# Kernel tuning notes

Hardware: AMD Instinct MI355X
Metric: run time of the kernel (lower is better)

The kernel has to match this reference:

```python
import jax, jax.numpy as jnp
import numpy as np

B, Hh, Ww, C, D = 32, 14, 14, 512, 8192

def setup_inputs() -> dict:
    key = jax.random.key(0)
    k1, k2, k3, k4, k5, k6 = jax.random.split(key, 6)
    bottom1 = jax.random.normal(k1, (B, Hh, Ww, C), dtype=jnp.float32)
    bottom2 = jax.random.normal(k2, (B, Hh, Ww, C), dtype=jnp.float32)
    # rand_s: random +/-1 (trainable weights in the original layer)
    rand_s_1 = (2.0 * jax.random.randint(k3, (C,), 0, 2).astype(jnp.float32) - 1.0)
    rand_s_2 = (2.0 * jax.random.randint(k4, (C,), 0, 2).astype(jnp.float32) - 1.0)
    # rand_h: hash bucket index in [0, D) per input channel (fixed, non-trainable)
    rand_h_1 = jax.random.randint(k5, (C,), 0, D, dtype=jnp.int32)
    rand_h_2 = jax.random.randint(k6, (C,), 0, D, dtype=jnp.int32)
    return {"bottom1": bottom1, "bottom2": bottom2,
            "rand_s_1": rand_s_1, "rand_s_2": rand_s_2,
            "rand_h_1": rand_h_1, "rand_h_2": rand_h_2}

def _count_sketch(x_flat, rand_s, rand_h, out_dim):
    # x_flat: [N, C]. Equivalent to x_flat @ sparse_sketch_matrix [C, out_dim]
    # where sketch[c, rand_h[c]] = rand_s[c].
    z = x_flat * rand_s                                   # [N, C]
    # scatter-add channels into their hash buckets along the feature axis
    return jax.ops.segment_sum(z.T, rand_h, num_segments=out_dim).T  # [N, D]

def reference(bottom1, bottom2, rand_s_1, rand_s_2, rand_h_1, rand_h_2):
    b, h, w, c1 = bottom1.shape
    c2 = bottom2.shape[-1]
    x1 = bottom1.reshape(-1, c1)
    x2 = bottom2.reshape(-1, c2)
    sk1 = _count_sketch(x1, rand_s_1, rand_h_1, D)        # [N, D]
    sk2 = _count_sketch(x2, rand_s_2, rand_h_2, D)        # [N, D]
    fft1 = jnp.fft.fft(sk1.astype(jnp.complex64), axis=-1)
    fft2 = jnp.fft.fft(sk2.astype(jnp.complex64), axis=-1)
    cbp_flat = jnp.real(jnp.fft.ifft(fft1 * fft2, axis=-1))  # circular conv
    cbp = cbp_flat.reshape(b, h, w, D)
    return jnp.sum(cbp, axis=(1, 2))                      # [B, D]
```

## Files before the change

kernel.cpp:

```cpp
#include <hip/hip_runtime.h>


#define NB   32
#define HW   196
#define CC   512
#define DD   8192
#define NTHR 256
#define TILES_PER_B 16

typedef __attribute__((ext_vector_type(8)))  __bf16 bf8;
typedef __attribute__((ext_vector_type(16))) float  f32x16;

__global__ __launch_bounds__(NTHR) void cbp_mfma_kernel(
    const float* __restrict__ x1, const float* __restrict__ x2,
    const float* __restrict__ s1, const float* __restrict__ s2,
    const int*   __restrict__ h1, const int*   __restrict__ h2,
    float* __restrict__ ws, float* __restrict__ out, int use_ws)
{
    __shared__ float accD[DD];

    const int bid  = blockIdx.x;
    const int b    = bid >> 4;
    const int t1   = (bid >> 2) & 3;
    const int t2   = bid & 3;
    const int tid  = threadIdx.x;
    const int wid  = tid >> 6;
    const int lane = tid & 63;
    const int wr   = wid >> 1;
    const int wc   = wid & 1;
    const int lo5  = lane & 31;
    const int hi   = lane >> 5;

    for (int i = tid; i < DD; i += NTHR) accD[i] = 0.0f;
    __syncthreads();

    const int c1w = t1 * 128 + wr * 64;
    const int c2w = t2 * 128 + wc * 64;

    const float* A0 = x1 + (size_t)b * HW * CC + (c1w + lo5);
    const float* A1 = A0 + 32;
    const float* B0 = x2 + (size_t)b * HW * CC + (c2w + lo5);
    const float* B1 = B0 + 32;

    f32x16 acc00 = {}, acc01 = {}, acc10 = {}, acc11 = {};

    for (int ks = 0; ks < 12; ++ks) {
        const int kb = ks * 16 + hi * 8;
        bf8 a0, a1, b0v, b1v;
        #pragma unroll
        for (int j = 0; j < 8; ++j) {
            const size_t off = (size_t)(kb + j) * CC;
            a0[j]  = (__bf16)A0[off];
            a1[j]  = (__bf16)A1[off];
            b0v[j] = (__bf16)B0[off];
            b1v[j] = (__bf16)B1[off];
        }
        acc00 = __builtin_amdgcn_mfma_f32_32x32x16_bf16(a0, b0v, acc00, 0, 0, 0);
        acc01 = __builtin_amdgcn_mfma_f32_32x32x16_bf16(a0, b1v, acc01, 0, 0, 0);
        acc10 = __builtin_amdgcn_mfma_f32_32x32x16_bf16(a1, b0v, acc10, 0, 0, 0);
        acc11 = __builtin_amdgcn_mfma_f32_32x32x16_bf16(a1, b1v, acc11, 0, 0, 0);
    }
    {
        const int kb = 192 + hi * 8;
        bf8 a0, a1, b0v, b1v;
        #pragma unroll
        for (int j = 0; j < 8; ++j) {
            const int k = kb + j;
            const size_t off = (size_t)k * CC;
            const bool v = (k < HW);
            a0[j]  = (__bf16)(v ? A0[off] : 0.0f);
            a1[j]  = (__bf16)(v ? A1[off] : 0.0f);
            b0v[j] = (__bf16)(v ? B0[off] : 0.0f);
            b1v[j] = (__bf16)(v ? B1[off] : 0.0f);
        }
        acc00 = __builtin_amdgcn_mfma_f32_32x32x16_bf16(a0, b0v, acc00, 0, 0, 0);
        acc01 = __builtin_amdgcn_mfma_f32_32x32x16_bf16(a0, b1v, acc01, 0, 0, 0);
        acc10 = __builtin_amdgcn_mfma_f32_32x32x16_bf16(a1, b0v, acc10, 0, 0, 0);
        acc11 = __builtin_amdgcn_mfma_f32_32x32x16_bf16(a1, b1v, acc11, 0, 0, 0);
    }

    const float s2v0 = s2[c2w + lo5];
    const float s2v1 = s2[c2w + 32 + lo5];
    const int   h2v0 = h2[c2w + lo5];
    const int   h2v1 = h2[c2w + 32 + lo5];

    #pragma unroll
    for (int rt = 0; rt < 2; ++rt) {
        const f32x16 accL = rt ? acc10 : acc00;
        const f32x16 accR = rt ? acc11 : acc01;
        #pragma unroll
        for (int reg = 0; reg < 16; ++reg) {
            const int c1 = c1w + rt * 32 + (reg & 3) + 8 * (reg >> 2) + 4 * hi;
            const float sv = s1[c1];
            const int   hv = h1[c1];
            atomicAdd(&accD[(hv + h2v0) & (DD - 1)], sv * s2v0 * accL[reg]);
            atomicAdd(&accD[(hv + h2v1) & (DD - 1)], sv * s2v1 * accR[reg]);
        }
    }
    __syncthreads();

    if (use_ws) {
        float4* dst = (float4*)(ws + (size_t)bid * DD);
        const float4* src = (const float4*)accD;
        #pragma unroll
        for (int i = 0; i < DD / 4 / NTHR; ++i)
            dst[tid + i * NTHR] = src[tid + i * NTHR];
    } else {
        float* ob = out + (size_t)b * DD;
        for (int i = tid; i < DD; i += NTHR)
            atomicAdd(&ob[i], accD[i]);
    }
}

__global__ __launch_bounds__(NTHR) void cbp_reduce_kernel(
    const float* __restrict__ ws, float* __restrict__ out)
{
    const int b   = blockIdx.x >> 3;
    const int d0  = (blockIdx.x & 7) * 1024 + threadIdx.x * 4;
    const float* base = ws + (size_t)b * TILES_PER_B * DD + d0;
    float4 sum = {0.f, 0.f, 0.f, 0.f};
    #pragma unroll
    for (int t = 0; t < TILES_PER_B; ++t) {
        float4 v = *(const float4*)(base + (size_t)t * DD);
        sum.x += v.x; sum.y += v.y; sum.z += v.z; sum.w += v.w;
    }
    *(float4*)(out + (size_t)b * DD + d0) = sum;
}

extern "C" void kernel_launch(void* const* d_in, const int* in_sizes, int n_in,
                              void* d_out, int out_size, void* d_ws, size_t ws_size,
                              hipStream_t stream) {
    const float* x1 = (const float*)d_in[0];
    const float* x2 = (const float*)d_in[1];
    const float* s1 = (const float*)d_in[2];
    const float* s2 = (const float*)d_in[3];
    const int*   h1 = (const int*)d_in[4];
    const int*   h2 = (const int*)d_in[5];
    float* out = (float*)d_out;
    float* ws  = (float*)d_ws;

    const size_t need = (size_t)NB * TILES_PER_B * DD * sizeof(float);
    const int use_ws = (ws_size >= need) ? 1 : 0;

    if (!use_ws) {
        hipMemsetAsync(out, 0, (size_t)out_size * sizeof(float), stream);
    }

    dim3 grid(NB * TILES_PER_B);
    dim3 block(NTHR);
    cbp_mfma_kernel<<<grid, block, 0, stream>>>(x1, x2, s1, s2, h1, h2, ws, out, use_ws);

    if (use_ws) {
        dim3 rgrid(NB * 8);
        cbp_reduce_kernel<<<rgrid, block, 0, stream>>>(ws, out);
    }
}
```

Baseline: 133.6 us.

## Pre-transpose inputs to padded bf16 channel-major layout before MFMA gram

```diff
diff --git a/kernel.cpp b/kernel.cpp
--- a/kernel.cpp
+++ b/kernel.cpp
@@ -5,17 +5,74 @@
 #define HW   196
 #define CC   512
 #define DD   8192
+#define KP   224
 #define NTHR 256
 #define TILES_PER_B 16
 
 typedef __attribute__((ext_vector_type(8)))  __bf16 bf8;
 typedef __attribute__((ext_vector_type(16))) float  f32x16;
 
-__global__ __launch_bounds__(NTHR) void cbp_mfma_kernel(
+#define XT_ELEMS ((size_t)NB * CC * KP)
+#define XT_BYTES (XT_ELEMS * 2)
+#define PART_OFF_BYTES (2 * XT_BYTES)
+#define PART_BYTES ((size_t)NB * TILES_PER_B * DD * 4)
+#define NEED_FAST (PART_OFF_BYTES + PART_BYTES)
+#define NEED_R5  PART_BYTES
+
+__global__ __launch_bounds__(NTHR) void cbp_transpose_kernel(
     const float* __restrict__ x1, const float* __restrict__ x2,
+    __bf16* __restrict__ xT1, __bf16* __restrict__ xT2)
+{
+    __shared__ float T[64][65];
+    const int bid = blockIdx.x;
+    const int b  = bid >> 5;
+    const int ct = (bid >> 2) & 7;
+    const int kt = bid & 3;
+    const int tid = threadIdx.x;
+
+    #pragma unroll
+    for (int m = 0; m < 2; ++m) {
+        const float* x   = m ? x2  : x1;
+        __bf16*      xTo = m ? xT2 : xT1;
+
+        #pragma unroll
+        for (int p = 0; p < 4; ++p) {
+            const int row  = p * 16 + (tid >> 4);
+            const int col4 = (tid & 15) * 4;
+            const int k = kt * 64 + row;
+            float4 v = {0.f, 0.f, 0.f, 0.f};
+            if (k < HW)
+                v = *(const float4*)(x + ((size_t)(b * HW + k) * CC + ct * 64 + col4));
+            T[col4 + 0][row] = v.x;
+            T[col4 + 1][row] = v.y;
+            T[col4 + 2][row] = v.z;
+            T[col4 + 3][row] = v.w;
+        }
+        __syncthreads();
+
+        const int c_l = tid >> 2;
+        const int seg = tid & 3;
+        const int kp0 = kt * 64 + seg * 16;
+        if (kp0 < KP) {
+            const size_t dstc = (size_t)(b * CC + ct * 64 + c_l) * KP;
+            #pragma unroll
+            for (int i2 = 0; i2 < 2; ++i2) {
+                bf8 v;
+                #pragma unroll
+                for (int i = 0; i < 8; ++i)
+                    v[i] = (__bf16)T[c_l][seg * 16 + i2 * 8 + i];
+                *(bf8*)(xTo + dstc + kp0 + i2 * 8) = v;
+            }
+        }
+        __syncthreads();
+    }
+}
+
+__global__ __launch_bounds__(NTHR) void cbp_gram_t_kernel(
+    const __bf16* __restrict__ xT1, const __bf16* __restrict__ xT2,
     const float* __restrict__ s1, const float* __restrict__ s2,
     const int*   __restrict__ h1, const int*   __restrict__ h2,
-    float* __restrict__ ws, float* __restrict__ out, int use_ws)
+    float* __restrict__ partials)
 {
     __shared__ float accD[DD];
 
@@ -37,23 +94,90 @@
     const int c1w = t1 * 128 + wr * 64;
     const int c2w = t2 * 128 + wc * 64;
 
+    const __bf16* A0 = xT1 + ((size_t)(b * CC + c1w + lo5) * KP + hi * 8);
+    const __bf16* A1 = A0 + (size_t)32 * KP;
+    const __bf16* B0 = xT2 + ((size_t)(b * CC + c2w + lo5) * KP + hi * 8);
+    const __bf16* B1 = B0 + (size_t)32 * KP;
+
+    f32x16 acc00 = {}, acc01 = {}, acc10 = {}, acc11 = {};
+
+    #pragma unroll
+    for (int ks = 0; ks < KP / 16; ++ks) {
+        const bf8 a0  = *(const bf8*)(A0 + ks * 16);
+        const bf8 a1  = *(const bf8*)(A1 + ks * 16);
+        const bf8 b0v = *(const bf8*)(B0 + ks * 16);
+        const bf8 b1v = *(const bf8*)(B1 + ks * 16);
+        acc00 = __builtin_amdgcn_mfma_f32_32x32x16_bf16(a0, b0v, acc00, 0, 0, 0);
+        acc01 = __builtin_amdgcn_mfma_f32_32x32x16_bf16(a0, b1v, acc01, 0, 0, 0);
+        acc10 = __builtin_amdgcn_mfma_f32_32x32x16_bf16(a1, b0v, acc10, 0, 0, 0);
+        acc11 = __builtin_amdgcn_mfma_f32_32x32x16_bf16(a1, b1v, acc11, 0, 0, 0);
+    }
+
+    const float s2v0 = s2[c2w + lo5];
+    const float s2v1 = s2[c2w + 32 + lo5];
+    const int   h2v0 = h2[c2w + lo5];
+    const int   h2v1 = h2[c2w + 32 + lo5];
+
+    #pragma unroll
+    for (int rt = 0; rt < 2; ++rt) {
+        const f32x16 accL = rt ? acc10 : acc00;
+        const f32x16 accR = rt ? acc11 : acc01;
+        #pragma unroll
+        for (int reg = 0; reg < 16; ++reg) {
+            const int c1 = c1w + rt * 32 + (reg & 3) + 8 * (reg >> 2) + 4 * hi;
+            const float sv = s1[c1];
+            const int   hv = h1[c1];
+            atomicAdd(&accD[(hv + h2v0) & (DD - 1)], sv * s2v0 * accL[reg]);
+            atomicAdd(&accD[(hv + h2v1) & (DD - 1)], sv * s2v1 * accR[reg]);
+        }
+    }
+    __syncthreads();
+
+    float4* dst = (float4*)(partials + (size_t)bid * DD);
+    const float4* src = (const float4*)accD;
+    #pragma unroll
+    for (int i = 0; i < DD / 4 / NTHR; ++i)
+        dst[tid + i * NTHR] = src[tid + i * NTHR];
+}
+
+__global__ __launch_bounds__(NTHR) void cbp_mfma_kernel(
+    const float* __restrict__ x1, const float* __restrict__ x2,
+    const float* __restrict__ s1, const float* __restrict__ s2,
+    const int*   __restrict__ h1, const int*   __restrict__ h2,
+    float* __restrict__ ws, float* __restrict__ out, int use_ws)
+{
+    __shared__ float accD[DD];
+    const int bid  = blockIdx.x;
+    const int b    = bid >> 4;
+    const int t1   = (bid >> 2) & 3;
+    const int t2   = bid & 3;
+    const int tid  = threadIdx.x;
+    const int wid  = tid >> 6;
+    const int lane = tid & 63;
+    const int wr   = wid >> 1;
+    const int wc   = wid & 1;
+    const int lo5  = lane & 31;
+    const int hi   = lane >> 5;
+
+    for (int i = tid; i < DD; i += NTHR) accD[i] = 0.0f;
+    __syncthreads();
+
+    const int c1w = t1 * 128 + wr * 64;
+    const int c2w = t2 * 128 + wc * 64;
     const float* A0 = x1 + (size_t)b * HW * CC + (c1w + lo5);
     const float* A1 = A0 + 32;
     const float* B0 = x2 + (size_t)b * HW * CC + (c2w + lo5);
     const float* B1 = B0 + 32;
 
     f32x16 acc00 = {}, acc01 = {}, acc10 = {}, acc11 = {};
-
     for (int ks = 0; ks < 12; ++ks) {
         const int kb = ks * 16 + hi * 8;
         bf8 a0, a1, b0v, b1v;
         #pragma unroll
         for (int j = 0; j < 8; ++j) {
             const size_t off = (size_t)(kb + j) * CC;
-            a0[j]  = (__bf16)A0[off];
-            a1[j]  = (__bf16)A1[off];
-            b0v[j] = (__bf16)B0[off];
-            b1v[j] = (__bf16)B1[off];
+            a0[j] = (__bf16)A0[off]; a1[j] = (__bf16)A1[off];
+            b0v[j] = (__bf16)B0[off]; b1v[j] = (__bf16)B1[off];
         }
         acc00 = __builtin_amdgcn_mfma_f32_32x32x16_bf16(a0, b0v, acc00, 0, 0, 0);
         acc01 = __builtin_amdgcn_mfma_f32_32x32x16_bf16(a0, b1v, acc01, 0, 0, 0);
@@ -83,7 +207,6 @@
     const float s2v1 = s2[c2w + 32 + lo5];
     const int   h2v0 = h2[c2w + lo5];
     const int   h2v1 = h2[c2w + 32 + lo5];
-
     #pragma unroll
     for (int rt = 0; rt < 2; ++rt) {
         const f32x16 accL = rt ? acc10 : acc00;
@@ -113,11 +236,11 @@
 }
 
 __global__ __launch_bounds__(NTHR) void cbp_reduce_kernel(
-    const float* __restrict__ ws, float* __restrict__ out)
-{
-    const int b   = blockIdx.x >> 3;
-    const int d0  = (blockIdx.x & 7) * 1024 + threadIdx.x * 4;
-    const float* base = ws + (size_t)b * TILES_PER_B * DD + d0;
+    const float* __restrict__ parts, float* __restrict__ out)
+{
+    const int b  = blockIdx.x >> 3;
+    const int d0 = (blockIdx.x & 7) * 1024 + threadIdx.x * 4;
+    const float* base = parts + (size_t)b * TILES_PER_B * DD + d0;
     float4 sum = {0.f, 0.f, 0.f, 0.f};
     #pragma unroll
     for (int t = 0; t < TILES_PER_B; ++t) {
@@ -137,21 +260,24 @@
     const int*   h1 = (const int*)d_in[4];
     const int*   h2 = (const int*)d_in[5];
     float* out = (float*)d_out;
-    float* ws  = (float*)d_ws;
-
-    const size_t need = (size_t)NB * TILES_PER_B * DD * sizeof(float);
-    const int use_ws = (ws_size >= need) ? 1 : 0;
-
-    if (!use_ws) {
+
+    dim3 block(NTHR);
+    if (ws_size >= NEED_FAST) {
+        __bf16* xT1 = (__bf16*)d_ws;
+        __bf16* xT2 = xT1 + XT_ELEMS;
+        float*  parts = (float*)((char*)d_ws + PART_OFF_BYTES);
+        cbp_transpose_kernel<<<dim3(NB * 32), block, 0, stream>>>(x1, x2, xT1, xT2);
+        cbp_gram_t_kernel<<<dim3(NB * TILES_PER_B), block, 0, stream>>>(
+            xT1, xT2, s1, s2, h1, h2, parts);
+        cbp_reduce_kernel<<<dim3(NB * 8), block, 0, stream>>>(parts, out);
+    } else if (ws_size >= NEED_R5) {
+        float* parts = (float*)d_ws;
+        cbp_mfma_kernel<<<dim3(NB * TILES_PER_B), block, 0, stream>>>(
+            x1, x2, s1, s2, h1, h2, parts, out, 1);
+        cbp_reduce_kernel<<<dim3(NB * 8), block, 0, stream>>>(parts, out);
+    } else {
         hipMemsetAsync(out, 0, (size_t)out_size * sizeof(float), stream);
-    }
-
-    dim3 grid(NB * TILES_PER_B);
-    dim3 block(NTHR);
-    cbp_mfma_kernel<<<grid, block, 0, stream>>>(x1, x2, s1, s2, h1, h2, ws, out, use_ws);
-
-    if (use_ws) {
-        dim3 rgrid(NB * 8);
-        cbp_reduce_kernel<<<rgrid, block, 0, stream>>>(ws, out);
-    }
-}
+        cbp_mfma_kernel<<<dim3(NB * TILES_PER_B), block, 0, stream>>>(
+            x1, x2, s1, s2, h1, h2, (float*)d_ws, out, 0);
+    }
+}
```

Result: slower. 143.1 us (+7.0%).
